# Optimization experiments

Hardware: AMD Instinct MI355X
Metric: run time of the kernel (lower is better)

Reference implementation:

```python
import jax, jax.numpy as jnp
import numpy as np

N = 33554432  # 2**25 elements
EPS = 1e-4    # keep probabilities strictly inside (0,1) to avoid log(0)

def setup_inputs() -> dict:
    key = jax.random.key(0)
    k1, k2 = jax.random.split(key)
    input_ = jax.random.uniform(k1, (N,), dtype=jnp.float32, minval=EPS, maxval=1.0 - EPS)
    target = jax.random.uniform(k2, (N,), dtype=jnp.float32, minval=EPS, maxval=1.0 - EPS)
    return {"input": input_, "target": target}

def reference(input, target):
    # Binary KL divergence per element, summed:
    # KL(p||q) = p*log(p/q) + (1-p)*log((1-p)/(1-q))
    p, q = input, target
    kl = p * (jnp.log(p) - jnp.log(q)) + (1.0 - p) * (jnp.log1p(-p) - jnp.log1p(-q))
    return kl.sum()
```

## Files before the change

kernel.cpp:

```cpp
#include <hip/hip_runtime.h>

#define BLOCK 256
#define GRID  2048

__device__ __forceinline__ float kl_elem(float p, float q) {
    float lp  = __logf(p);
    float lq  = __logf(q);
    float l1p = __logf(1.0f - p);
    float l1q = __logf(1.0f - q);
    return p * (lp - lq) + (1.0f - p) * (l1p - l1q);
}

__global__ __launch_bounds__(BLOCK) void kl_div_kernel(
        const float* __restrict__ p,
        const float* __restrict__ q,
        float* __restrict__ out,
        int n) {
    const int nvec = n >> 2;
    const float4* __restrict__ p4 = reinterpret_cast<const float4*>(p);
    const float4* __restrict__ q4 = reinterpret_cast<const float4*>(q);

    float acc = 0.0f;
    const int stride = gridDim.x * blockDim.x;
    for (int i = blockIdx.x * blockDim.x + threadIdx.x; i < nvec; i += stride) {
        float4 pv = p4[i];
        float4 qv = q4[i];
        acc += kl_elem(pv.x, qv.x);
        acc += kl_elem(pv.y, qv.y);
        acc += kl_elem(pv.z, qv.z);
        acc += kl_elem(pv.w, qv.w);
    }
    for (int i = (nvec << 2) + blockIdx.x * blockDim.x + threadIdx.x; i < n; i += stride) {
        acc += kl_elem(p[i], q[i]);
    }

    #pragma unroll
    for (int off = 32; off > 0; off >>= 1)
        acc += __shfl_down(acc, off, 64);

    __shared__ float wave_sums[BLOCK / 64];
    const int lane = threadIdx.x & 63;
    const int wave = threadIdx.x >> 6;
    if (lane == 0) wave_sums[wave] = acc;
    __syncthreads();

    if (threadIdx.x == 0) {
        float s = 0.0f;
        #pragma unroll
        for (int w = 0; w < BLOCK / 64; ++w) s += wave_sums[w];
        atomicAdd(out, s);
    }
}

extern "C" void kernel_launch(void* const* d_in, const int* in_sizes, int n_in,
                              void* d_out, int out_size, void* d_ws, size_t ws_size,
                              hipStream_t stream) {
    const float* p = (const float*)d_in[0];
    const float* q = (const float*)d_in[1];
    float* out = (float*)d_out;
    const int n = in_sizes[0];

    hipMemsetAsync(out, 0, sizeof(float), stream);

    kl_div_kernel<<<GRID, BLOCK, 0, stream>>>(p, q, out, n);
}
```

Measured before the change: 282.0 us.

## Specialize fully unrolled batched-load kernel with log2 math and split accumulators

Adds a fast path used when n exactly equals grid*block*16*4. In that path each thread issues batches of four float4 loads for both inputs before computing, which raises memory-level parallelism, and it spreads the sums over four independent accumulators. The per-element math now uses log2 with fmaf and applies a single ln2 scale per block instead of natural logs per element. The fast path depends on the input size matching the hardcoded grid shape; other sizes fall back to the generic kernel.

```diff
diff --git a/kernel.cpp b/kernel.cpp
--- a/kernel.cpp
+++ b/kernel.cpp
@@ -2,38 +2,20 @@
 
 #define BLOCK 256
 #define GRID  2048
+#define VPT   16
+#define BATCH 4
 
-__device__ __forceinline__ float kl_elem(float p, float q) {
-    float lp  = __logf(p);
-    float lq  = __logf(q);
-    float l1p = __logf(1.0f - p);
-    float l1q = __logf(1.0f - q);
-    return p * (lp - lq) + (1.0f - p) * (l1p - l1q);
+__device__ __forceinline__ void kl_acc(float p, float q, float& acc) {
+    float omp = 1.0f - p;
+    float omq = 1.0f - q;
+    float d1  = __log2f(p)   - __log2f(q);
+    float d2  = __log2f(omp) - __log2f(omq);
+    acc = fmaf(p,   d1, acc);
+    acc = fmaf(omp, d2, acc);
 }
 
-__global__ __launch_bounds__(BLOCK) void kl_div_kernel(
-        const float* __restrict__ p,
-        const float* __restrict__ q,
-        float* __restrict__ out,
-        int n) {
-    const int nvec = n >> 2;
-    const float4* __restrict__ p4 = reinterpret_cast<const float4*>(p);
-    const float4* __restrict__ q4 = reinterpret_cast<const float4*>(q);
-
-    float acc = 0.0f;
-    const int stride = gridDim.x * blockDim.x;
-    for (int i = blockIdx.x * blockDim.x + threadIdx.x; i < nvec; i += stride) {
-        float4 pv = p4[i];
-        float4 qv = q4[i];
-        acc += kl_elem(pv.x, qv.x);
-        acc += kl_elem(pv.y, qv.y);
-        acc += kl_elem(pv.z, qv.z);
-        acc += kl_elem(pv.w, qv.w);
-    }
-    for (int i = (nvec << 2) + blockIdx.x * blockDim.x + threadIdx.x; i < n; i += stride) {
-        acc += kl_elem(p[i], q[i]);
-    }
-
+__device__ __forceinline__ void block_reduce_and_atomic(float acc, float* out) {
+    const float LN2 = 0.69314718055994530942f;
     #pragma unroll
     for (int off = 32; off > 0; off >>= 1)
         acc += __shfl_down(acc, off, 64);
@@ -48,8 +30,64 @@
         float s = 0.0f;
         #pragma unroll
         for (int w = 0; w < BLOCK / 64; ++w) s += wave_sums[w];
-        atomicAdd(out, s);
+        atomicAdd(out, s * LN2);
     }
+}
+
+__global__ __launch_bounds__(BLOCK, 8) void kl_div_fast(
+        const float4* __restrict__ p4,
+        const float4* __restrict__ q4,
+        float* __restrict__ out) {
+    const int gid = blockIdx.x * BLOCK + threadIdx.x;
+    const int stride = GRID * BLOCK;
+
+    float acc0 = 0.0f, acc1 = 0.0f, acc2 = 0.0f, acc3 = 0.0f;
+
+    #pragma unroll
+    for (int b = 0; b < VPT / BATCH; ++b) {
+        float4 pv[BATCH], qv[BATCH];
+        #pragma unroll
+        for (int k = 0; k < BATCH; ++k) {
+            const int i = gid + (b * BATCH + k) * stride;
+            pv[k] = p4[i];
+            qv[k] = q4[i];
+        }
+        #pragma unroll
+        for (int k = 0; k < BATCH; ++k) {
+            kl_acc(pv[k].x, qv[k].x, acc0);
+            kl_acc(pv[k].y, qv[k].y, acc1);
+            kl_acc(pv[k].z, qv[k].z, acc2);
+            kl_acc(pv[k].w, qv[k].w, acc3);
+        }
+    }
+
+    float acc = (acc0 + acc1) + (acc2 + acc3);
+    block_reduce_and_atomic(acc, out);
+}
+
+__global__ __launch_bounds__(BLOCK) void kl_div_generic(
+        const float* __restrict__ p,
+        const float* __restrict__ q,
+        float* __restrict__ out,
+        int n) {
+    const int nvec = n >> 2;
+    const float4* __restrict__ p4 = reinterpret_cast<const float4*>(p);
+    const float4* __restrict__ q4 = reinterpret_cast<const float4*>(q);
+
+    float acc = 0.0f;
+    const int stride = gridDim.x * blockDim.x;
+    for (int i = blockIdx.x * blockDim.x + threadIdx.x; i < nvec; i += stride) {
+        float4 pv = p4[i];
+        float4 qv = q4[i];
+        kl_acc(pv.x, qv.x, acc);
+        kl_acc(pv.y, qv.y, acc);
+        kl_acc(pv.z, qv.z, acc);
+        kl_acc(pv.w, qv.w, acc);
+    }
+    for (int i = (nvec << 2) + blockIdx.x * blockDim.x + threadIdx.x; i < n; i += stride) {
+        kl_acc(p[i], q[i], acc);
+    }
+    block_reduce_and_atomic(acc, out);
 }
 
 extern "C" void kernel_launch(void* const* d_in, const int* in_sizes, int n_in,
@@ -62,5 +100,11 @@
 
     hipMemsetAsync(out, 0, sizeof(float), stream);
 
-    kl_div_kernel<<<GRID, BLOCK, 0, stream>>>(p, q, out, n);
+    if (n == GRID * BLOCK * VPT * 4) {
+        kl_div_fast<<<GRID, BLOCK, 0, stream>>>(
+            reinterpret_cast<const float4*>(p),
+            reinterpret_cast<const float4*>(q), out);
+    } else {
+        kl_div_generic<<<GRID, BLOCK, 0, stream>>>(p, q, out, n);
+    }
 }
```

New measurement: 272.7 us. -3.3%, faster.
